# Optimization experiments

Measured on AMD Instinct MI355X. Metric: run time of the kernel, lower is better.

The kernel has to match this reference:

```python
import jax, jax.numpy as jnp
import numpy as np

# BitLinear follows the BitNet b1.58 recipe used by fla's HGRN-Bit:
#   x -> RMSNorm(no weight) -> per-token int8 activation quant (STE)
#   w -> ternary quant with global mean-abs scale (STE)
#   out = x_q @ w_q.T

def _rms_norm(x, eps=1e-8, weight=None):
    var = jnp.mean(x * x, axis=-1, keepdims=True)
    y = x * jax.lax.rsqrt(var + eps)
    return y * weight if weight is not None else y


def _act_quant(x):
    # per-token absmax int8 quant-dequant with straight-through estimator
    scale = 127.0 / jnp.clip(jnp.max(jnp.abs(x), axis=-1, keepdims=True), 1e-5, None)
    q = jnp.clip(jnp.round(x * scale), -128, 127) / scale
    return x + jax.lax.stop_gradient(q - x)


def _weight_quant(w):
    # ternary {-1,0,1} quant-dequant with global mean-abs scale, STE
    scale = 1.0 / jnp.clip(jnp.mean(jnp.abs(w)), 1e-5, None)
    q = jnp.clip(jnp.round(w * scale), -1, 1) / scale
    return w + jax.lax.stop_gradient(q - w)


def _bit_linear(x, w):
    xq = _act_quant(_rms_norm(x))
    wq = _weight_quant(w)
    return jnp.einsum('...i,oi->...o', xq, wq)


def setup_inputs() -> dict:
    key = jax.random.key(0)
    ks = jax.random.split(key, 5)
    B, S = 2, 4096
    D_IN = 4096           # input_dim == 2 * hidden_size
    H = 2048              # hidden_size
    INTER = 2 * H         # HGRNBitMLP intermediate_size = hidden_size*2 = 4096
    condition = jax.random.normal(ks[0], (B, S, D_IN), dtype=jnp.float32)
    w_gate = jax.random.normal(ks[1], (2 * INTER, D_IN), dtype=jnp.float32) * 0.02   # [8192,4096]
    w_down = jax.random.normal(ks[2], (D_IN, INTER), dtype=jnp.float32) * 0.02        # [4096,4096]
    norm_weight = jnp.ones((2 * H,), dtype=jnp.float32)                                # RMSNorm(hidden_size*2)
    w_out = jax.random.normal(ks[3], (2 * H, 2 * H), dtype=jnp.float32) * 0.02         # [4096,4096]
    return {"condition": condition, "w_gate": w_gate, "w_down": w_down,
            "norm_weight": norm_weight, "w_out": w_out}


def reference(condition, w_gate, w_down, norm_weight, w_out):
    # HGRNBitMLP: gate_proj -> chunk -> swiglu -> down_proj
    y = _bit_linear(condition, w_gate)              # [B,S,8192]
    gate, v = jnp.split(y, 2, axis=-1)              # each [B,S,4096]
    h = _bit_linear(gate * jax.nn.sigmoid(gate) * v, w_down)  # swiglu then down, [B,S,4096]
    # AdaLN head: RMSNorm (learned weight) then quantized out projection
    h = _rms_norm(h, eps=1e-6, weight=norm_weight)
    params = _bit_linear(h, w_out)                  # [B,S,4096]
    scale, shift = jnp.split(params, 2, axis=-1)    # each [B,S,2048]
    return (scale, shift)
```

## Files before the change

### kernel.cpp

```cpp
#include <hip/hip_runtime.h>
#include <hip/hip_bf16.h>

typedef int i32x4 __attribute__((ext_vector_type(4)));
typedef signed char i8;


__device__ __forceinline__ void gload_lds16(const void* g, void* l) {
  __builtin_amdgcn_global_load_lds(
      (const __attribute__((address_space(1))) unsigned int*)g,
      (__attribute__((address_space(3))) unsigned int*)l, 16, 0, 0);
}

__device__ __forceinline__ float wmean_clip(const double* p, double cnt) {
  double m = *p / cnt;
  if (m < 1e-5) m = 1e-5;
  return (float)m;
}

__device__ __forceinline__ float blk_sum(float v, float* s4) {
  for (int m = 32; m; m >>= 1) v += __shfl_xor(v, m);
  if ((threadIdx.x & 63) == 0) s4[threadIdx.x >> 6] = v;
  __syncthreads();
  float r = s4[0] + s4[1] + s4[2] + s4[3];
  __syncthreads();
  return r;
}

__device__ __forceinline__ float blk_max(float v, float* s4) {
  for (int m = 32; m; m >>= 1) v = fmaxf(v, __shfl_xor(v, m));
  if ((threadIdx.x & 63) == 0) s4[threadIdx.x >> 6] = v;
  __syncthreads();
  float r = fmaxf(fmaxf(s4[0], s4[1]), fmaxf(s4[2], s4[3]));
  __syncthreads();
  return r;
}

__device__ __forceinline__ void xcd_swz(int gx, int& bm, int& bn) {
  const int nwg = gx * gridDim.y;
  const int o = blockIdx.y * gx + blockIdx.x;
  const int s = (o & 7) * (nwg >> 3) + (o >> 3);
  bm = s / gx;
  bn = s % gx;
}


__global__ __launch_bounds__(256) void wabs_all(
    const float* __restrict__ W0, const float* __restrict__ W1,
    const float* __restrict__ W2, double* __restrict__ sums) {
  __shared__ double s4[4];
  const int b = blockIdx.x;
  const float4* W4;
  size_t n4;
  int rb, nb, r;
  if (b < 1024) { r = 0; rb = b; nb = 1024; W4 = (const float4*)W0; n4 = (size_t)8192 * 1024; }
  else if (b < 1536) { r = 1; rb = b - 1024; nb = 512; W4 = (const float4*)W1; n4 = (size_t)4096 * 1024; }
  else { r = 2; rb = b - 1536; nb = 512; W4 = (const float4*)W2; n4 = (size_t)4096 * 1024; }
  size_t i = (size_t)rb * 256 + threadIdx.x;
  size_t stride = (size_t)nb * 256;
  double s = 0.0;
  for (; i < n4; i += stride) {
    float4 v = W4[i];
    s += (double)fabsf(v.x);
    s += (double)fabsf(v.y);
    s += (double)fabsf(v.z);
    s += (double)fabsf(v.w);
  }
  for (int m = 32; m; m >>= 1) s += __shfl_xor(s, m);
  if ((threadIdx.x & 63) == 0) s4[threadIdx.x >> 6] = s;
  __syncthreads();
  if (threadIdx.x == 0) atomicAdd(&sums[r], s4[0] + s4[1] + s4[2] + s4[3]);
}


__global__ __launch_bounds__(256) void wquant_all(
    const float* __restrict__ W0, const float* __restrict__ W1,
    const float* __restrict__ W2, i8* __restrict__ Q0, i8* __restrict__ Q1,
    i8* __restrict__ Q2, const double* __restrict__ sums) {
  const int b = blockIdx.x;
  const float4* W4;
  i8* Q;
  size_t n4;
  int rb, nb, r;
  double cnt;
  if (b < 2048) { r = 0; rb = b; nb = 2048; W4 = (const float4*)W0; Q = Q0; n4 = (size_t)8192 * 1024; cnt = 33554432.0; }
  else if (b < 3072) { r = 1; rb = b - 2048; nb = 1024; W4 = (const float4*)W1; Q = Q1; n4 = (size_t)4096 * 1024; cnt = 16777216.0; }
  else { r = 2; rb = b - 3072; nb = 1024; W4 = (const float4*)W2; Q = Q2; n4 = (size_t)4096 * 1024; cnt = 16777216.0; }
  const float scale = 1.0f / wmean_clip(&sums[r], cnt);
  size_t i = (size_t)rb * 256 + threadIdx.x;
  size_t stride = (size_t)nb * 256;
  for (; i < n4; i += stride) {
    float4 v = W4[i];
    char4 o;
    o.x = (i8)fminf(fmaxf(rintf(v.x * scale), -1.f), 1.f);
    o.y = (i8)fminf(fmaxf(rintf(v.y * scale), -1.f), 1.f);
    o.z = (i8)fminf(fmaxf(rintf(v.z * scale), -1.f), 1.f);
    o.w = (i8)fminf(fmaxf(rintf(v.w * scale), -1.f), 1.f);
    *(char4*)&Q[i * 4] = o;
  }
}


template <bool HEAD>
__global__ __launch_bounds__(256) void rowquant(
    const float* __restrict__ X, const float* __restrict__ nw,
    i8* __restrict__ Aq, float* __restrict__ rowscale, float eps1) {
  __shared__ float s4[4];
  const int t = threadIdx.x;
  const size_t base = (size_t)blockIdx.x * 4096;
  float x[16];
#pragma unroll
  for (int c = 0; c < 4; ++c) {
    float4 v = *(const float4*)&X[base + c * 1024 + t * 4];
    x[c * 4 + 0] = v.x; x[c * 4 + 1] = v.y;
    x[c * 4 + 2] = v.z; x[c * 4 + 3] = v.w;
  }
  float ss = 0.f;
#pragma unroll
  for (int i = 0; i < 16; ++i) ss += x[i] * x[i];
  ss = blk_sum(ss, s4);
  float inv = 1.0f / sqrtf(ss * (1.0f / 4096.0f) + eps1);
  if (HEAD) {
#pragma unroll
    for (int c = 0; c < 4; ++c) {
      float4 w = *(const float4*)&nw[c * 1024 + t * 4];
      x[c * 4 + 0] = x[c * 4 + 0] * inv * w.x;
      x[c * 4 + 1] = x[c * 4 + 1] * inv * w.y;
      x[c * 4 + 2] = x[c * 4 + 2] * inv * w.z;
      x[c * 4 + 3] = x[c * 4 + 3] * inv * w.w;
    }
    float ss2 = 0.f;
#pragma unroll
    for (int i = 0; i < 16; ++i) ss2 += x[i] * x[i];
    ss2 = blk_sum(ss2, s4);
    inv = 1.0f / sqrtf(ss2 * (1.0f / 4096.0f) + 1e-8f);
  }
#pragma unroll
  for (int i = 0; i < 16; ++i) x[i] = x[i] * inv;
  float amax = 0.f;
#pragma unroll
  for (int i = 0; i < 16; ++i) amax = fmaxf(amax, fabsf(x[i]));
  amax = blk_max(amax, s4);
  float cs = fmaxf(amax, 1e-5f);
  float sx = 127.0f / cs;
#pragma unroll
  for (int c = 0; c < 4; ++c) {
    char4 o;
    o.x = (i8)fminf(fmaxf(rintf(x[c * 4 + 0] * sx), -128.f), 127.f);
    o.y = (i8)fminf(fmaxf(rintf(x[c * 4 + 1] * sx), -128.f), 127.f);
    o.z = (i8)fminf(fmaxf(rintf(x[c * 4 + 2] * sx), -128.f), 127.f);
    o.w = (i8)fminf(fmaxf(rintf(x[c * 4 + 3] * sx), -128.f), 127.f);
    *(char4*)&Aq[base + c * 1024 + t * 4] = o;
  }
  if (t == 0) rowscale[blockIdx.x] = cs / 127.0f;
}


__global__ __launch_bounds__(256) void gemm1_fused(
    const i8* __restrict__ A, const i8* __restrict__ Wg,
    float* __restrict__ SW, const float* __restrict__ rowscale,
    const double* __restrict__ wsum) {
  const int K = 4096;
  __shared__ i8 As[2][8192];
  __shared__ i8 Bg[2][4096];
  __shared__ i8 Bv[2][4096];
  const int t = threadIdx.x;
  int bmi, bni;
  xcd_swz(64, bmi, bni);
  const int bm0 = bmi * 128, bn0 = bni * 64;
  const int lane = t & 63, wave = t >> 6;
  const int wr = wave >> 1, wc = wave & 1;

  i32x4 accg[4][2] = {};
  i32x4 accv[4][2] = {};

  const i8* gA = A + (size_t)(bm0 + (t & 127)) * K + (t >> 7) * 16;
  const i8* gG = Wg + (size_t)(bn0 + (t & 63)) * K + (t >> 6) * 16;
  const i8* gV = Wg + (size_t)(4096 + bn0 + (t & 63)) * K + (t >> 6) * 16;

  auto stage = [&](int buf, int kt) {
    gload_lds16(gA + kt, &As[buf][t * 16]);
    gload_lds16(gA + kt + 32, &As[buf][4096 + t * 16]);
    gload_lds16(gG + kt, &Bg[buf][t * 16]);
    gload_lds16(gV + kt, &Bv[buf][t * 16]);
  };

  stage(0, 0);
  __syncthreads();

  const int ar = wr * 64 + (lane & 15);
  const int br = wc * 32 + (lane & 15);
  const int kcA = (lane >> 4) * 2048;
  const int kcB = (lane >> 4) * 1024;

  int cur = 0;
  for (int kt = 0; kt < K; kt += 64) {
    if (kt + 64 < K) stage(cur ^ 1, kt + 64);
    i32x4 af[4], bg[2], bv[2];
#pragma unroll
    for (int m = 0; m < 4; ++m) af[m] = *(const i32x4*)&As[cur][kcA + (ar + m * 16) * 16];
#pragma unroll
    for (int n = 0; n < 2; ++n) {
      bg[n] = *(const i32x4*)&Bg[cur][kcB + (br + n * 16) * 16];
      bv[n] = *(const i32x4*)&Bv[cur][kcB + (br + n * 16) * 16];
    }
#pragma unroll
    for (int m = 0; m < 4; ++m)
#pragma unroll
      for (int n = 0; n < 2; ++n) {
        accg[m][n] = __builtin_amdgcn_mfma_i32_16x16x64_i8(af[m], bg[n], accg[m][n], 0, 0, 0);
        accv[m][n] = __builtin_amdgcn_mfma_i32_16x16x64_i8(af[m], bv[n], accv[m][n], 0, 0, 0);
      }
    __syncthreads();
    cur ^= 1;
  }

  const float cm = wmean_clip(wsum, 33554432.0);
#pragma unroll
  for (int m = 0; m < 4; ++m) {
    const int r0 = bm0 + wr * 64 + m * 16 + (lane >> 4) * 4;
#pragma unroll
    for (int j = 0; j < 4; ++j) {
      const int row = r0 + j;
      const float f = rowscale[row] * cm;
#pragma unroll
      for (int n = 0; n < 2; ++n) {
        const int col = bn0 + wc * 32 + n * 16 + (lane & 15);
        float g = (float)accg[m][n][j] * f;
        float v = (float)accv[m][n][j] * f;
        float s = g / (1.0f + expf(-g)) * v;
        SW[(size_t)row * 4096 + col] = s;
      }
    }
  }
}


template <int EPI>
__global__ __launch_bounds__(256) void gemm_bt(
    const i8* __restrict__ A, const i8* __restrict__ B,
    float* __restrict__ C, const float* __restrict__ rowscale,
    const double* __restrict__ wsum, double wcnt, int M) {
  const int K = 4096, N = 4096;
  __shared__ i8 As[2][8192];
  __shared__ i8 Bs[2][8192];
  const int t = threadIdx.x;
  int bmi, bni;
  xcd_swz(32, bmi, bni);
  const int bm0 = bmi * 128, bn0 = bni * 128;
  const int lane = t & 63, wave = t >> 6;
  const int wr = wave >> 1, wc = wave & 1;

  i32x4 acc[4][4] = {};

  const i8* gA = A + (size_t)(bm0 + (t & 127)) * K + (t >> 7) * 16;
  const i8* gB = B + (size_t)(bn0 + (t & 127)) * K + (t >> 7) * 16;

  auto stage = [&](int buf, int kt) {
    gload_lds16(gA + kt, &As[buf][t * 16]);
    gload_lds16(gA + kt + 32, &As[buf][4096 + t * 16]);
    gload_lds16(gB + kt, &Bs[buf][t * 16]);
    gload_lds16(gB + kt + 32, &Bs[buf][4096 + t * 16]);
  };

  stage(0, 0);
  __syncthreads();

  const int ar = wr * 64 + (lane & 15);
  const int br = wc * 64 + (lane & 15);
  const int kc = (lane >> 4) * 2048;

  int cur = 0;
  for (int kt = 0; kt < K; kt += 64) {
    if (kt + 64 < K) stage(cur ^ 1, kt + 64);
    i32x4 af[4], bfr[4];
#pragma unroll
    for (int m = 0; m < 4; ++m) af[m] = *(const i32x4*)&As[cur][kc + (ar + m * 16) * 16];
#pragma unroll
    for (int n = 0; n < 4; ++n) bfr[n] = *(const i32x4*)&Bs[cur][kc + (br + n * 16) * 16];
#pragma unroll
    for (int m = 0; m < 4; ++m)
#pragma unroll
      for (int n = 0; n < 4; ++n)
        acc[m][n] = __builtin_amdgcn_mfma_i32_16x16x64_i8(af[m], bfr[n], acc[m][n], 0, 0, 0);
    __syncthreads();
    cur ^= 1;
  }

  const float cm = wmean_clip(wsum, wcnt);
#pragma unroll
  for (int m = 0; m < 4; ++m) {
    const int r0 = bm0 + wr * 64 + m * 16 + (lane >> 4) * 4;
#pragma unroll
    for (int j = 0; j < 4; ++j) {
      const int row = r0 + j;
      const float f = rowscale[row] * cm;
#pragma unroll
      for (int n = 0; n < 4; ++n) {
        const int col = bn0 + wc * 64 + n * 16 + (lane & 15);
        const float val = (float)acc[m][n][j] * f;
        if (EPI == 0) {
          C[(size_t)row * N + col] = val;
        } else {
          if (col < 2048)
            C[(size_t)row * 2048 + col] = val;
          else
            C[(size_t)M * 2048 + (size_t)row * 2048 + (col - 2048)] = val;
        }
      }
    }
  }
}


extern "C" void kernel_launch(void* const* d_in, const int* in_sizes, int n_in,
                              void* d_out, int out_size, void* d_ws, size_t ws_size,
                              hipStream_t stream) {
  const float* cond = (const float*)d_in[0];
  const float* w_gate = (const float*)d_in[1];
  const float* w_down = (const float*)d_in[2];
  const float* norm_w = (const float*)d_in[3];
  const float* w_out = (const float*)d_in[4];
  float* out = (float*)d_out;

  const int M = in_sizes[0] / 4096;

  char* ws = (char*)d_ws;
  double* sums = (double*)ws;
  i8* wq_gate = (i8*)(ws + 256);
  i8* wq_down = wq_gate + (size_t)8192 * 4096;
  i8* wq_out = wq_down + (size_t)4096 * 4096;
  i8* Aq = wq_out + (size_t)4096 * 4096;
  float* rowscale = (float*)(Aq + (size_t)M * 4096);
  float* act = rowscale + 8192;

  hipMemsetAsync(sums, 0, 3 * sizeof(double), stream);

  wabs_all<<<2048, 256, 0, stream>>>(w_gate, w_down, w_out, sums);
  wquant_all<<<4096, 256, 0, stream>>>(w_gate, w_down, w_out, wq_gate, wq_down, wq_out, sums);

  rowquant<false><<<M, 256, 0, stream>>>(cond, nullptr, Aq, rowscale, 1e-8f);
  gemm1_fused<<<dim3(4096 / 64, M / 128), 256, 0, stream>>>(Aq, wq_gate, act, rowscale, &sums[0]);

  rowquant<false><<<M, 256, 0, stream>>>(act, nullptr, Aq, rowscale, 1e-8f);
  gemm_bt<0><<<dim3(4096 / 128, M / 128), 256, 0, stream>>>(Aq, wq_down, act, rowscale, &sums[1], 16777216.0, M);

  rowquant<true><<<M, 256, 0, stream>>>(act, norm_w, Aq, rowscale, 1e-6f);
  gemm_bt<1><<<dim3(4096 / 128, M / 128), 256, 0, stream>>>(Aq, wq_out, out, rowscale, &sums[2], 16777216.0, M);
}
```

Before: 1.639 ms.

## Triple-buffer int8 GEMM LDS staging with explicit vmcnt waits and barriers

Both int8 GEMM kernels move from double to triple LDS buffering, issuing global-to-LDS loads two tiles ahead. Partial vmcnt waits replace the full __syncthreads drain, so one tile's loads stay in flight while another is consumed. MFMA sections are wrapped in s_setprio to favour matrix issue. The cost is more LDS per block (48KB vs 32KB), which may reduce occupancy, plus extra barriers per iteration.

```diff
diff --git a/kernel.cpp b/kernel.cpp
--- a/kernel.cpp
+++ b/kernel.cpp
@@ -3,6 +3,10 @@
 
 typedef int i32x4 __attribute__((ext_vector_type(4)));
 typedef signed char i8;
+
+#define VMCNT(n) asm volatile("s_waitcnt vmcnt(" #n ")" ::: "memory")
+#define SBAR() asm volatile("s_barrier" ::: "memory")
+#define SCHEDB() __builtin_amdgcn_sched_barrier(0)
 
 
 __device__ __forceinline__ void gload_lds16(const void* g, void* l) {
@@ -159,10 +163,9 @@
     const i8* __restrict__ A, const i8* __restrict__ Wg,
     float* __restrict__ SW, const float* __restrict__ rowscale,
     const double* __restrict__ wsum) {
-  const int K = 4096;
-  __shared__ i8 As[2][8192];
-  __shared__ i8 Bg[2][4096];
-  __shared__ i8 Bv[2][4096];
+  const int K = 4096, NT = 64;
+  __shared__ i8 As[3 * 8192];
+  __shared__ i8 Bs[3 * 8192];
   const int t = threadIdx.x;
   int bmi, bni;
   xcd_swz(64, bmi, bni);
@@ -177,32 +180,43 @@
   const i8* gG = Wg + (size_t)(bn0 + (t & 63)) * K + (t >> 6) * 16;
   const i8* gV = Wg + (size_t)(4096 + bn0 + (t & 63)) * K + (t >> 6) * 16;
 
-  auto stage = [&](int buf, int kt) {
-    gload_lds16(gA + kt, &As[buf][t * 16]);
-    gload_lds16(gA + kt + 32, &As[buf][4096 + t * 16]);
-    gload_lds16(gG + kt, &Bg[buf][t * 16]);
-    gload_lds16(gV + kt, &Bv[buf][t * 16]);
+  auto stage = [&](int so, int kt) {
+    gload_lds16(gA + kt, &As[so + t * 16]);
+    gload_lds16(gA + kt + 32, &As[so + 4096 + t * 16]);
+    gload_lds16(gG + kt, &Bs[so + t * 16]);
+    gload_lds16(gV + kt, &Bs[so + 4096 + t * 16]);
   };
 
   stage(0, 0);
-  __syncthreads();
-
-  const int ar = wr * 64 + (lane & 15);
-  const int br = wc * 32 + (lane & 15);
+  stage(8192, 64);
+
+  const int arow = (wr * 64 + (lane & 15)) * 16;
+  const int brow = (wc * 32 + (lane & 15)) * 16;
   const int kcA = (lane >> 4) * 2048;
   const int kcB = (lane >> 4) * 1024;
 
-  int cur = 0;
-  for (int kt = 0; kt < K; kt += 64) {
-    if (kt + 64 < K) stage(cur ^ 1, kt + 64);
+  int cso = 0, pso = 16384;
+  for (int j = 0; j < NT; ++j) {
+    if (j + 2 < NT) {
+      stage(pso, (j + 2) * 64);
+      VMCNT(8);
+    } else if (j + 1 < NT) {
+      VMCNT(4);
+    } else {
+      VMCNT(0);
+    }
+    SCHEDB();
+    SBAR();
+    SCHEDB();
     i32x4 af[4], bg[2], bv[2];
 #pragma unroll
-    for (int m = 0; m < 4; ++m) af[m] = *(const i32x4*)&As[cur][kcA + (ar + m * 16) * 16];
+    for (int m = 0; m < 4; ++m) af[m] = *(const i32x4*)&As[cso + kcA + arow + m * 256];
 #pragma unroll
     for (int n = 0; n < 2; ++n) {
-      bg[n] = *(const i32x4*)&Bg[cur][kcB + (br + n * 16) * 16];
-      bv[n] = *(const i32x4*)&Bv[cur][kcB + (br + n * 16) * 16];
-    }
+      bg[n] = *(const i32x4*)&Bs[cso + kcB + brow + n * 256];
+      bv[n] = *(const i32x4*)&Bs[cso + 4096 + kcB + brow + n * 256];
+    }
+    __builtin_amdgcn_s_setprio(1);
 #pragma unroll
     for (int m = 0; m < 4; ++m)
 #pragma unroll
@@ -210,8 +224,12 @@
         accg[m][n] = __builtin_amdgcn_mfma_i32_16x16x64_i8(af[m], bg[n], accg[m][n], 0, 0, 0);
         accv[m][n] = __builtin_amdgcn_mfma_i32_16x16x64_i8(af[m], bv[n], accv[m][n], 0, 0, 0);
       }
-    __syncthreads();
-    cur ^= 1;
+    __builtin_amdgcn_s_setprio(0);
+    SCHEDB();
+    SBAR();
+    SCHEDB();
+    cso = (cso == 16384) ? 0 : cso + 8192;
+    pso = (pso == 16384) ? 0 : pso + 8192;
   }
 
   const float cm = wmean_clip(wsum, 33554432.0);
@@ -240,9 +258,9 @@
     const i8* __restrict__ A, const i8* __restrict__ B,
     float* __restrict__ C, const float* __restrict__ rowscale,
     const double* __restrict__ wsum, double wcnt, int M) {
-  const int K = 4096, N = 4096;
-  __shared__ i8 As[2][8192];
-  __shared__ i8 Bs[2][8192];
+  const int K = 4096, N = 4096, NT = 64;
+  __shared__ i8 As[3 * 8192];
+  __shared__ i8 Bs[3 * 8192];
   const int t = threadIdx.x;
   int bmi, bni;
   xcd_swz(32, bmi, bni);
@@ -255,35 +273,50 @@
   const i8* gA = A + (size_t)(bm0 + (t & 127)) * K + (t >> 7) * 16;
   const i8* gB = B + (size_t)(bn0 + (t & 127)) * K + (t >> 7) * 16;
 
-  auto stage = [&](int buf, int kt) {
-    gload_lds16(gA + kt, &As[buf][t * 16]);
-    gload_lds16(gA + kt + 32, &As[buf][4096 + t * 16]);
-    gload_lds16(gB + kt, &Bs[buf][t * 16]);
-    gload_lds16(gB + kt + 32, &Bs[buf][4096 + t * 16]);
+  auto stage = [&](int so, int kt) {
+    gload_lds16(gA + kt, &As[so + t * 16]);
+    gload_lds16(gA + kt + 32, &As[so + 4096 + t * 16]);
+    gload_lds16(gB + kt, &Bs[so + t * 16]);
+    gload_lds16(gB + kt + 32, &Bs[so + 4096 + t * 16]);
   };
 
   stage(0, 0);
-  __syncthreads();
-
-  const int ar = wr * 64 + (lane & 15);
-  const int br = wc * 64 + (lane & 15);
+  stage(8192, 64);
+
+  const int arow = (wr * 64 + (lane & 15)) * 16;
+  const int brow = (wc * 64 + (lane & 15)) * 16;
   const int kc = (lane >> 4) * 2048;
 
-  int cur = 0;
-  for (int kt = 0; kt < K; kt += 64) {
-    if (kt + 64 < K) stage(cur ^ 1, kt + 64);
+  int cso = 0, pso = 16384;
+  for (int j = 0; j < NT; ++j) {
+    if (j + 2 < NT) {
+      stage(pso, (j + 2) * 64);
+      VMCNT(8);
+    } else if (j + 1 < NT) {
+      VMCNT(4);
+    } else {
+      VMCNT(0);
+    }
+    SCHEDB();
+    SBAR();
+    SCHEDB();
     i32x4 af[4], bfr[4];
 #pragma unroll
-    for (int m = 0; m < 4; ++m) af[m] = *(const i32x4*)&As[cur][kc + (ar + m * 16) * 16];
-#pragma unroll
-    for (int n = 0; n < 4; ++n) bfr[n] = *(const i32x4*)&Bs[cur][kc + (br + n * 16) * 16];
+    for (int m = 0; m < 4; ++m) af[m] = *(const i32x4*)&As[cso + kc + arow + m * 256];
+#pragma unroll
+    for (int n = 0; n < 4; ++n) bfr[n] = *(const i32x4*)&Bs[cso + kc + brow + n * 256];
+    __builtin_amdgcn_s_setprio(1);
 #pragma unroll
     for (int m = 0; m < 4; ++m)
 #pragma unroll
       for (int n = 0; n < 4; ++n)
         acc[m][n] = __builtin_amdgcn_mfma_i32_16x16x64_i8(af[m], bfr[n], acc[m][n], 0, 0, 0);
-    __syncthreads();
-    cur ^= 1;
+    __builtin_amdgcn_s_setprio(0);
+    SCHEDB();
+    SBAR();
+    SCHEDB();
+    cso = (cso == 16384) ? 0 : cso + 8192;
+    pso = (pso == 16384) ? 0 : pso + 8192;
   }
 
   const float cm = wmean_clip(wsum, wcnt);
```

Result: no change. 1.642 ms (+0.1%).
